# Kernel tuning notes

Measured on AMD Instinct MI355X. Metric: run time of the kernel, lower is better.

Reference implementation:

```python
import jax, jax.numpy as jnp
import numpy as np
import math

D_MODEL = 1024
NHEAD = 16
D_K = D_MODEL // NHEAD
B, S = 2, 2048


def setup_inputs() -> dict:
    key = jax.random.key(0)
    ks = jax.random.split(key, 9)
    x = jax.random.normal(ks[0], (B, S, D_MODEL), dtype=jnp.float32)
    # causal mask, broadcastable to (B, nhead, S, S); 0 entries are masked out
    mask = jnp.tril(jnp.ones((S, S), dtype=jnp.int32))[None, None, :, :]
    scale = 1.0 / math.sqrt(D_MODEL)
    def lin(kw, kb):
        W = jax.random.uniform(kw, (D_MODEL, D_MODEL), dtype=jnp.float32, minval=-scale, maxval=scale)
        b = jax.random.uniform(kb, (D_MODEL,), dtype=jnp.float32, minval=-scale, maxval=scale)
        return W, b
    Wq, bq = lin(ks[1], ks[2])
    Wk, bk = lin(ks[3], ks[4])
    Wv, bv = lin(ks[5], ks[6])
    Wo, bo = lin(ks[7], ks[8])
    return {"x": x, "mask": mask, "Wq": Wq, "bq": bq, "Wk": Wk, "bk": bk,
            "Wv": Wv, "bv": bv, "Wo": Wo, "bo": bo}


def reference(x, mask, Wq, bq, Wk, bk, Wv, bv, Wo, bo):
    b, s, _ = x.shape
    def heads(W, bias):
        # (b, s, d_model) @ (d_model, d_model) -> (b, nhead, s, d_k)
        return (x @ W.T + bias).reshape(b, s, NHEAD, D_K).transpose(0, 2, 1, 3)
    Q, K, V = heads(Wq, bq), heads(Wk, bk), heads(Wv, bv)
    scores = jnp.einsum('bhqd,bhkd->bhqk', Q, K) / math.sqrt(D_K)
    scores = jnp.where(mask == 0, jnp.float32(-1e9), scores)
    attn = jax.nn.softmax(scores, axis=-1)  # dropout is identity in eval mode
    out = jnp.einsum('bhqk,bhkd->bhqd', attn, V)
    out = out.transpose(0, 2, 1, 3).reshape(b, s, D_MODEL)
    return out @ Wo.T + bo
```

## Files before the change

kernel.cpp:

```cpp
#include <hip/hip_runtime.h>
#include <hip/hip_bf16.h>

#define DMODEL 1024
#define NH     16
#define DKH    64
#define BSZ    2
#define SEQ    2048
#define MROWS  (BSZ*SEQ)
#define WELEM  (DMODEL*DMODEL)

typedef __attribute__((ext_vector_type(8))) short short8;
typedef __attribute__((ext_vector_type(4))) float f32x4;

__device__ __forceinline__ ushort f2bf(float f) {
    return __bfloat16_as_ushort(__float2bfloat16(f));
}
__device__ __forceinline__ unsigned pk2(float lo, float hi) {
    return (unsigned)f2bf(lo) | ((unsigned)f2bf(hi) << 16);
}

__global__ __launch_bounds__(256)
void cvt_all(const float* __restrict__ x,
             const float* __restrict__ W0, const float* __restrict__ W1,
             const float* __restrict__ W2, const float* __restrict__ W3,
             ushort* __restrict__ xbf, ushort* __restrict__ Wcat,
             ushort* __restrict__ Wo)
{
    const int blk = blockIdx.x;
    const float* src;
    ushort* dst;
    int base;
    if (blk < 2048)      { src = x;  dst = xbf;             base = blk * 2048; }
    else if (blk < 2560) { src = W0; dst = Wcat;            base = (blk - 2048) * 2048; }
    else if (blk < 3072) { src = W1; dst = Wcat + WELEM;    base = (blk - 2560) * 2048; }
    else if (blk < 3584) { src = W2; dst = Wcat + 2*WELEM;  base = (blk - 3072) * 2048; }
    else                 { src = W3; dst = Wo;              base = (blk - 3584) * 2048; }
    const size_t off = (size_t)base + threadIdx.x * 8;
    const float4 f0 = *(const float4*)(src + off);
    const float4 f1 = *(const float4*)(src + off + 4);
    uint4 o;
    o.x = pk2(f0.x, f0.y); o.y = pk2(f0.z, f0.w);
    o.z = pk2(f1.x, f1.y); o.w = pk2(f1.z, f1.w);
    *(uint4*)(dst + off) = o;
}

__global__ __launch_bounds__(256)
void gemm_qkv(const ushort* __restrict__ xbf, const ushort* __restrict__ Wcat,
              const float* __restrict__ bq, const float* __restrict__ bk,
              const float* __restrict__ bv,
              ushort* __restrict__ Qh, ushort* __restrict__ Kh,
              ushort* __restrict__ VT)
{
    __shared__ ushort Ash[128][40];
    __shared__ ushort Bsh[128][40];

    const int t    = threadIdx.x;
    const int m0   = blockIdx.y * 128, n0 = blockIdx.x * 128;
    const int srow = t >> 1;
    const int shal = (t & 1) * 16;

    const int wave = t >> 6;
    const int lane = t & 63;
    const int wr   = (wave >> 1) * 64;
    const int wc   = (wave & 1) * 64;
    const int quad = lane >> 4;
    const int r16  = lane & 15;

    f32x4 acc[4][4];
    #pragma unroll
    for (int i = 0; i < 4; ++i)
        #pragma unroll
        for (int j = 0; j < 4; ++j)
            acc[i][j] = (f32x4){0.f, 0.f, 0.f, 0.f};

    for (int k0 = 0; k0 < DMODEL; k0 += 32) {
        const ushort* ap = xbf  + (size_t)(m0 + srow) * DMODEL + k0 + shal;
        const ushort* wp = Wcat + (size_t)(n0 + srow) * DMODEL + k0 + shal;
        *(uint4*)&Ash[srow][shal]     = *(const uint4*)(ap);
        *(uint4*)&Ash[srow][shal + 8] = *(const uint4*)(ap + 8);
        *(uint4*)&Bsh[srow][shal]     = *(const uint4*)(wp);
        *(uint4*)&Bsh[srow][shal + 8] = *(const uint4*)(wp + 8);
        __syncthreads();

        short8 af[4], bf[4];
        #pragma unroll
        for (int i = 0; i < 4; ++i) af[i] = *(const short8*)&Ash[wr + i * 16 + r16][quad * 8];
        #pragma unroll
        for (int j = 0; j < 4; ++j) bf[j] = *(const short8*)&Bsh[wc + j * 16 + r16][quad * 8];

        #pragma unroll
        for (int i = 0; i < 4; ++i)
            #pragma unroll
            for (int j = 0; j < 4; ++j)
                acc[i][j] = __builtin_amdgcn_mfma_f32_16x16x32_bf16(af[i], bf[j], acc[i][j], 0, 0, 0);
        __syncthreads();
    }

    const int region = n0 >> 10;
    const float* bp  = (region == 0) ? bq : (region == 1) ? bk : bv;
    ushort* outQK    = (region == 0) ? Qh : Kh;
    const float osc  = (region == 0) ? 0.125f : 1.0f;
    const int nbase  = n0 & 1023;

    #pragma unroll
    for (int i = 0; i < 4; ++i) {
        #pragma unroll
        for (int j = 0; j < 4; ++j) {
            #pragma unroll
            for (int reg = 0; reg < 4; ++reg) {
                const int m  = m0 + wr + i * 16 + quad * 4 + reg;
                const int n  = nbase + wc + j * 16 + r16;
                const float v = (acc[i][j][reg] + bp[n]) * osc;
                const int b = m >> 11, s = m & (SEQ - 1);
                const int h = n >> 6,  dk = n & 63;
                if (region < 2) {
                    outQK[((size_t)(b * NH + h) * SEQ + s) * DKH + dk] = f2bf(v);
                } else {
                    VT[(((size_t)(b * NH + h)) * DKH + dk) * SEQ + s] = f2bf(v);
                }
            }
        }
    }
}

__global__ __launch_bounds__(256)
void gemm_out(const ushort* __restrict__ O, const ushort* __restrict__ Wo,
              const float* __restrict__ bo, float* __restrict__ out)
{
    __shared__ ushort Ash[128][40];
    __shared__ ushort Bsh[64][40];

    const int t    = threadIdx.x;
    const int m0   = blockIdx.y * 128, n0 = blockIdx.x * 64;
    const int wave = t >> 6;
    const int lane = t & 63;
    const int wr   = (wave >> 1) * 64;
    const int wc   = (wave & 1) * 32;
    const int quad = lane >> 4;
    const int r16  = lane & 15;

    f32x4 acc[4][2];
    #pragma unroll
    for (int i = 0; i < 4; ++i)
        #pragma unroll
        for (int j = 0; j < 2; ++j)
            acc[i][j] = (f32x4){0.f, 0.f, 0.f, 0.f};

    for (int k0 = 0; k0 < DMODEL; k0 += 32) {
        {
            const int srow = t >> 1, shal = (t & 1) * 16;
            const int m = m0 + srow;
            const ushort* ap = O + ((size_t)(m >> 11) * NH + (k0 >> 6)) * (SEQ * DKH)
                                 + (size_t)(m & (SEQ - 1)) * DKH + (k0 & 63) + shal;
            *(uint4*)&Ash[srow][shal]     = *(const uint4*)(ap);
            *(uint4*)&Ash[srow][shal + 8] = *(const uint4*)(ap + 8);
        }
        {
            const int brow = t >> 2, bc = (t & 3) * 8;
            const ushort* wp = Wo + (size_t)(n0 + brow) * DMODEL + k0 + bc;
            *(uint4*)&Bsh[brow][bc] = *(const uint4*)(wp);
        }
        __syncthreads();

        short8 af[4], bf[2];
        #pragma unroll
        for (int i = 0; i < 4; ++i) af[i] = *(const short8*)&Ash[wr + i * 16 + r16][quad * 8];
        #pragma unroll
        for (int j = 0; j < 2; ++j) bf[j] = *(const short8*)&Bsh[wc + j * 16 + r16][quad * 8];

        #pragma unroll
        for (int i = 0; i < 4; ++i)
            #pragma unroll
            for (int j = 0; j < 2; ++j)
                acc[i][j] = __builtin_amdgcn_mfma_f32_16x16x32_bf16(af[i], bf[j], acc[i][j], 0, 0, 0);
        __syncthreads();
    }

    #pragma unroll
    for (int i = 0; i < 4; ++i) {
        #pragma unroll
        for (int j = 0; j < 2; ++j) {
            #pragma unroll
            for (int reg = 0; reg < 4; ++reg) {
                const int m = m0 + wr + i * 16 + quad * 4 + reg;
                const int n = n0 + wc + j * 16 + r16;
                out[(size_t)m * DMODEL + n] = acc[i][j][reg] + bo[n];
            }
        }
    }
}

__global__ __launch_bounds__(256)
void gemm_mfma(const void* __restrict__ A, const void* __restrict__ W,
               const float* __restrict__ bias, void* __restrict__ out,
               int amode, int bmode, int outmode, float oscale)
{
    __shared__ ushort Ash[128][40];
    __shared__ ushort Bsh[128][40];

    const int t    = threadIdx.x;
    const int m0   = blockIdx.y * 128, n0 = blockIdx.x * 128;
    const int srow = t >> 1;
    const int shal = (t & 1) * 16;

    const int wave = t >> 6;
    const int lane = t & 63;
    const int wr   = (wave >> 1) * 64;
    const int wc   = (wave & 1) * 64;
    const int quad = lane >> 4;
    const int r16  = lane & 15;

    f32x4 acc[4][4];
    #pragma unroll
    for (int i = 0; i < 4; ++i)
        #pragma unroll
        for (int j = 0; j < 4; ++j)
            acc[i][j] = (f32x4){0.f, 0.f, 0.f, 0.f};

    for (int k0 = 0; k0 < DMODEL; k0 += 32) {
        uint4 a01, a23, b01, b23;
        if (amode == 0) {
            const float* ap = (const float*)A + (size_t)(m0 + srow) * DMODEL + k0 + shal;
            const float4 f0 = *(const float4*)(ap);
            const float4 f1 = *(const float4*)(ap + 4);
            const float4 f2 = *(const float4*)(ap + 8);
            const float4 f3 = *(const float4*)(ap + 12);
            a01 = (uint4){pk2(f0.x,f0.y), pk2(f0.z,f0.w), pk2(f1.x,f1.y), pk2(f1.z,f1.w)};
            a23 = (uint4){pk2(f2.x,f2.y), pk2(f2.z,f2.w), pk2(f3.x,f3.y), pk2(f3.z,f3.w)};
        } else if (amode == 1) {
            const int m = m0 + srow;
            const ushort* ap = (const ushort*)A
                + ((size_t)(m >> 11) * NH + (k0 >> 6)) * (SEQ * DKH)
                + (size_t)(m & (SEQ - 1)) * DKH + (k0 & 63) + shal;
            a01 = *(const uint4*)(ap);
            a23 = *(const uint4*)(ap + 8);
        } else {
            const ushort* ap = (const ushort*)A + (size_t)(m0 + srow) * DMODEL + k0 + shal;
            a01 = *(const uint4*)(ap);
            a23 = *(const uint4*)(ap + 8);
        }
        if (bmode == 0) {
            const float* wp = (const float*)W + (size_t)(n0 + srow) * DMODEL + k0 + shal;
            const float4 w0 = *(const float4*)(wp);
            const float4 w1 = *(const float4*)(wp + 4);
            const float4 w2 = *(const float4*)(wp + 8);
            const float4 w3 = *(const float4*)(wp + 12);
            b01 = (uint4){pk2(w0.x,w0.y), pk2(w0.z,w0.w), pk2(w1.x,w1.y), pk2(w1.z,w1.w)};
            b23 = (uint4){pk2(w2.x,w2.y), pk2(w2.z,w2.w), pk2(w3.x,w3.y), pk2(w3.z,w3.w)};
        } else {
            const ushort* wp = (const ushort*)W + (size_t)(n0 + srow) * DMODEL + k0 + shal;
            b01 = *(const uint4*)(wp);
            b23 = *(const uint4*)(wp + 8);
        }

        *(uint4*)&Ash[srow][shal]     = a01;
        *(uint4*)&Ash[srow][shal + 8] = a23;
        *(uint4*)&Bsh[srow][shal]     = b01;
        *(uint4*)&Bsh[srow][shal + 8] = b23;
        __syncthreads();

        short8 af[4], bf[4];
        #pragma unroll
        for (int i = 0; i < 4; ++i) af[i] = *(const short8*)&Ash[wr + i * 16 + r16][quad * 8];
        #pragma unroll
        for (int j = 0; j < 4; ++j) bf[j] = *(const short8*)&Bsh[wc + j * 16 + r16][quad * 8];

        #pragma unroll
        for (int i = 0; i < 4; ++i)
            #pragma unroll
            for (int j = 0; j < 4; ++j)
                acc[i][j] = __builtin_amdgcn_mfma_f32_16x16x32_bf16(af[i], bf[j], acc[i][j], 0, 0, 0);
        __syncthreads();
    }

    #pragma unroll
    for (int i = 0; i < 4; ++i) {
        #pragma unroll
        for (int j = 0; j < 4; ++j) {
            #pragma unroll
            for (int reg = 0; reg < 4; ++reg) {
                const int m = m0 + wr + i * 16 + quad * 4 + reg;
                const int n = n0 + wc + j * 16 + r16;
                const float v = (acc[i][j][reg] + bias[n]) * oscale;
                if (outmode == 0) {
                    ((float*)out)[(size_t)m * DMODEL + n] = v;
                } else if (outmode == 1) {
                    ((ushort*)out)[((size_t)(m >> 11) * NH + (n >> 6)) * (SEQ * DKH)
                                   + (size_t)(m & (SEQ - 1)) * DKH + (n & 63)] = f2bf(v);
                } else {
                    ((ushort*)out)[(((size_t)(m >> 11) * NH + (n >> 6)) * DKH + (n & 63)) * SEQ
                                   + (m & (SEQ - 1))] = f2bf(v);
                }
            }
        }
    }
}

__global__ __launch_bounds__(256)
void attn_flash(ushort* __restrict__ Qh,
                const ushort* __restrict__ Kh,
                const ushort* __restrict__ VT)
{
    __shared__ ushort Kl[128][72];
    __shared__ ushort Vl[64][136];
    __shared__ ushort Pl[4][16][136];

    const int t256 = threadIdx.x;
    const int wave = t256 >> 6;
    const int lane = t256 & 63;
    const int quad = lane >> 4;
    const int r16  = lane & 15;

    const int slot = blockIdx.x & 7;
    const int rest = blockIdx.x >> 3;
    const int bh   = slot * 4 + (rest & 3);
    const int p    = rest >> 2;

    ushort*       Qbase = Qh + (size_t)bh * SEQ * DKH;
    const ushort* Kbase = Kh + (size_t)bh * SEQ * DKH;
    const ushort* Vbase = VT + (size_t)bh * DKH * SEQ;

    #pragma unroll
    for (int pass = 0; pass < 2; ++pass) {
        const int qt = pass ? (31 - p) : p;
        const int q0 = qt * 64;

        short8 qf[2];
        {
            const ushort* qrow = Qbase + (size_t)(q0 + wave * 16 + r16) * DKH;
            qf[0] = *(const short8*)(qrow + quad * 8);
            qf[1] = *(const short8*)(qrow + 32 + quad * 8);
        }

        f32x4 oacc[4];
        #pragma unroll
        for (int i = 0; i < 4; ++i) oacc[i] = (f32x4){0.f, 0.f, 0.f, 0.f};
        float lpart[4] = {0.f, 0.f, 0.f, 0.f};

        const int T   = (qt >> 1) + 1;
        const int off = (qt & 1) * 64;

        for (int t = 0; t < T; ++t) {
            {
                const int krow = t256 >> 1, kc = (t256 & 1) * 32;
                const ushort* kg = Kbase + (size_t)(t * 128 + krow) * DKH + kc;
                *(uint4*)&Kl[krow][kc]      = *(const uint4*)(kg);
                *(uint4*)&Kl[krow][kc + 8]  = *(const uint4*)(kg + 8);
                *(uint4*)&Kl[krow][kc + 16] = *(const uint4*)(kg + 16);
                *(uint4*)&Kl[krow][kc + 24] = *(const uint4*)(kg + 24);
                const int vrow = t256 >> 2, vc = (t256 & 3) * 32;
                const ushort* vg = Vbase + (size_t)vrow * SEQ + t * 128 + vc;
                *(uint4*)&Vl[vrow][vc]      = *(const uint4*)(vg);
                *(uint4*)&Vl[vrow][vc + 8]  = *(const uint4*)(vg + 8);
                *(uint4*)&Vl[vrow][vc + 16] = *(const uint4*)(vg + 16);
                *(uint4*)&Vl[vrow][vc + 24] = *(const uint4*)(vg + 24);
            }
            __syncthreads();

            f32x4 sacc[8];
            #pragma unroll
            for (int nt = 0; nt < 8; ++nt) {
                sacc[nt] = (f32x4){0.f, 0.f, 0.f, 0.f};
                short8 b0 = *(const short8*)&Kl[nt * 16 + r16][quad * 8];
                short8 b1 = *(const short8*)&Kl[nt * 16 + r16][32 + quad * 8];
                sacc[nt] = __builtin_amdgcn_mfma_f32_16x16x32_bf16(qf[0], b0, sacc[nt], 0, 0, 0);
                sacc[nt] = __builtin_amdgcn_mfma_f32_16x16x32_bf16(qf[1], b1, sacc[nt], 0, 0, 0);
            }

            const bool diag = (t == T - 1);
            #pragma unroll
            for (int reg = 0; reg < 4; ++reg) {
                const int row_local = wave * 16 + quad * 4 + reg + off;
                #pragma unroll
                for (int nt = 0; nt < 8; ++nt) {
                    float pv = __expf(sacc[nt][reg]);
                    if (diag && (nt * 16 + r16) > row_local) pv = 0.f;
                    lpart[reg] += pv;
                    Pl[wave][quad * 4 + reg][nt * 16 + r16] = f2bf(pv);
                }
            }

            #pragma unroll
            for (int c = 0; c < 4; ++c) {
                short8 af = *(const short8*)&Pl[wave][r16][c * 32 + quad * 8];
                #pragma unroll
                for (int ct = 0; ct < 4; ++ct) {
                    short8 bf = *(const short8*)&Vl[ct * 16 + r16][c * 32 + quad * 8];
                    oacc[ct] = __builtin_amdgcn_mfma_f32_16x16x32_bf16(af, bf, oacc[ct], 0, 0, 0);
                }
            }
            __syncthreads();
        }

        #pragma unroll
        for (int reg = 0; reg < 4; ++reg)
            for (int d = 1; d < 16; d <<= 1)
                lpart[reg] += __shfl_xor(lpart[reg], d, 64);

        #pragma unroll
        for (int reg = 0; reg < 4; ++reg) {
            const float inv = 1.f / lpart[reg];
            const int q = q0 + wave * 16 + quad * 4 + reg;
            ushort* orow = Qbase + (size_t)q * DKH;
            #pragma unroll
            for (int ct = 0; ct < 4; ++ct)
                orow[ct * 16 + r16] = f2bf(oacc[ct][reg] * inv);
        }
        __syncthreads();
    }
}

extern "C" void kernel_launch(void* const* d_in, const int* in_sizes, int n_in,
                              void* d_out, int out_size, void* d_ws, size_t ws_size,
                              hipStream_t stream)
{
    const float* x  = (const float*)d_in[0];
    const float* Wf[4] = {(const float*)d_in[2], (const float*)d_in[4],
                          (const float*)d_in[6], (const float*)d_in[8]};
    const float* Bf[4] = {(const float*)d_in[3], (const float*)d_in[5],
                          (const float*)d_in[7], (const float*)d_in[9]};

    const size_t HSZ = (size_t)MROWS * DMODEL;
    ushort* Qh = (ushort*)d_ws;
    ushort* Kh = (ushort*)d_out;
    ushort* VT = (ushort*)d_out + HSZ;

    const dim3 blk(256);

    if (ws_size >= 24u * 1024 * 1024) {
        ushort* Wcat = Qh + HSZ;
        ushort* Wo   = Wcat + 3 * (size_t)WELEM;
        ushort* xbf  = Wo + WELEM;

        cvt_all<<<dim3(4096), blk, 0, stream>>>(x, Wf[0], Wf[1], Wf[2], Wf[3],
                                                xbf, Wcat, Wo);

        gemm_qkv<<<dim3(3 * DMODEL / 128, MROWS / 128), blk, 0, stream>>>(
            xbf, Wcat, Bf[0], Bf[1], Bf[2], Qh, Kh, VT);

        attn_flash<<<dim3(BSZ * NH * 16), blk, 0, stream>>>(Qh, Kh, VT);

        gemm_out<<<dim3(DMODEL / 64, MROWS / 128), blk, 0, stream>>>(
            Qh, Wo, Bf[3], (float*)d_out);
    } else {
        const dim3 gg(DMODEL / 128, MROWS / 128);
        gemm_mfma<<<gg, blk, 0, stream>>>(x, Wf[0], Bf[0], Qh, 0, 0, 1, 0.125f);
        gemm_mfma<<<gg, blk, 0, stream>>>(x, Wf[1], Bf[1], Kh, 0, 0, 1, 1.0f);
        gemm_mfma<<<gg, blk, 0, stream>>>(x, Wf[2], Bf[2], VT, 0, 0, 2, 1.0f);
        attn_flash<<<dim3(BSZ * NH * 16), blk, 0, stream>>>(Qh, Kh, VT);
        gemm_mfma<<<gg, blk, 0, stream>>>(Qh, Wf[3], Bf[3], d_out, 1, 0, 0, 1.0f);
    }
}
```

Baseline: 217.3 us.

## Use direct global-to-LDS loads in GEMMs and one query tile per attention block

Both GEMM kernels now stage their tiles with global_load_lds, which writes global memory straight into LDS without passing through registers. The LDS rows lose their padding, so the MFMA fragment reads may hit more bank conflicts. Separately, the attention kernel drops the paired-pass scheme where each block handled tile p and tile 31-p. It now launches twice as many blocks, one query tile each, trading the old load balancing for more parallelism and fewer registers live across passes.

```diff
diff --git a/kernel.cpp b/kernel.cpp
--- a/kernel.cpp
+++ b/kernel.cpp
@@ -17,6 +17,11 @@
 }
 __device__ __forceinline__ unsigned pk2(float lo, float hi) {
     return (unsigned)f2bf(lo) | ((unsigned)f2bf(hi) << 16);
+}
+__device__ __forceinline__ void load_lds16(const ushort* g, ushort* l) {
+    __builtin_amdgcn_global_load_lds(
+        (const __attribute__((address_space(1))) unsigned int*)g,
+        (__attribute__((address_space(3))) unsigned int*)l, 16, 0, 0);
 }
 
 __global__ __launch_bounds__(256)
@@ -51,14 +56,11 @@
               ushort* __restrict__ Qh, ushort* __restrict__ Kh,
               ushort* __restrict__ VT)
 {
-    __shared__ ushort Ash[128][40];
-    __shared__ ushort Bsh[128][40];
+    __shared__ ushort Ash[128][32];
+    __shared__ ushort Bsh[128][32];
 
     const int t    = threadIdx.x;
     const int m0   = blockIdx.y * 128, n0 = blockIdx.x * 128;
-    const int srow = t >> 1;
-    const int shal = (t & 1) * 16;
-
     const int wave = t >> 6;
     const int lane = t & 63;
     const int wr   = (wave >> 1) * 64;
@@ -66,6 +68,10 @@
     const int quad = lane >> 4;
     const int r16  = lane & 15;
 
+    const int row0 = wave * 16 + (lane >> 2);
+    const int row1 = 64 + wave * 16 + (lane >> 2);
+    const int ch   = (lane & 3) * 8;
+
     f32x4 acc[4][4];
     #pragma unroll
     for (int i = 0; i < 4; ++i)
@@ -74,12 +80,10 @@
             acc[i][j] = (f32x4){0.f, 0.f, 0.f, 0.f};
 
     for (int k0 = 0; k0 < DMODEL; k0 += 32) {
-        const ushort* ap = xbf  + (size_t)(m0 + srow) * DMODEL + k0 + shal;
-        const ushort* wp = Wcat + (size_t)(n0 + srow) * DMODEL + k0 + shal;
-        *(uint4*)&Ash[srow][shal]     = *(const uint4*)(ap);
-        *(uint4*)&Ash[srow][shal + 8] = *(const uint4*)(ap + 8);
-        *(uint4*)&Bsh[srow][shal]     = *(const uint4*)(wp);
-        *(uint4*)&Bsh[srow][shal + 8] = *(const uint4*)(wp + 8);
+        load_lds16(xbf  + (size_t)(m0 + row0) * DMODEL + k0 + ch, &Ash[wave * 16][0]);
+        load_lds16(xbf  + (size_t)(m0 + row1) * DMODEL + k0 + ch, &Ash[64 + wave * 16][0]);
+        load_lds16(Wcat + (size_t)(n0 + row0) * DMODEL + k0 + ch, &Bsh[wave * 16][0]);
+        load_lds16(Wcat + (size_t)(n0 + row1) * DMODEL + k0 + ch, &Bsh[64 + wave * 16][0]);
         __syncthreads();
 
         short8 af[4], bf[4];
@@ -127,8 +131,8 @@
 void gemm_out(const ushort* __restrict__ O, const ushort* __restrict__ Wo,
               const float* __restrict__ bo, float* __restrict__ out)
 {
-    __shared__ ushort Ash[128][40];
-    __shared__ ushort Bsh[64][40];
+    __shared__ ushort Ash[128][32];
+    __shared__ ushort Bsh[64][32];
 
     const int t    = threadIdx.x;
     const int m0   = blockIdx.y * 128, n0 = blockIdx.x * 64;
@@ -139,6 +143,10 @@
     const int quad = lane >> 4;
     const int r16  = lane & 15;
 
+    const int row0 = wave * 16 + (lane >> 2);
+    const int row1 = 64 + wave * 16 + (lane >> 2);
+    const int ch   = (lane & 3) * 8;
+
     f32x4 acc[4][2];
     #pragma unroll
     for (int i = 0; i < 4; ++i)
@@ -147,19 +155,14 @@
             acc[i][j] = (f32x4){0.f, 0.f, 0.f, 0.f};
 
     for (int k0 = 0; k0 < DMODEL; k0 += 32) {
-        {
-            const int srow = t >> 1, shal = (t & 1) * 16;
-            const int m = m0 + srow;
-            const ushort* ap = O + ((size_t)(m >> 11) * NH + (k0 >> 6)) * (SEQ * DKH)
-                                 + (size_t)(m & (SEQ - 1)) * DKH + (k0 & 63) + shal;
-            *(uint4*)&Ash[srow][shal]     = *(const uint4*)(ap);
-            *(uint4*)&Ash[srow][shal + 8] = *(const uint4*)(ap + 8);
-        }
-        {
-            const int brow = t >> 2, bc = (t & 3) * 8;
-            const ushort* wp = Wo + (size_t)(n0 + brow) * DMODEL + k0 + bc;
-            *(uint4*)&Bsh[brow][bc] = *(const uint4*)(wp);
-        }
+        const int ma0 = m0 + row0, ma1 = m0 + row1;
+        load_lds16(O + ((size_t)(ma0 >> 11) * NH + (k0 >> 6)) * (SEQ * DKH)
+                     + (size_t)(ma0 & (SEQ - 1)) * DKH + (k0 & 63) + ch,
+                   &Ash[wave * 16][0]);
+        load_lds16(O + ((size_t)(ma1 >> 11) * NH + (k0 >> 6)) * (SEQ * DKH)
+                     + (size_t)(ma1 & (SEQ - 1)) * DKH + (k0 & 63) + ch,
+                   &Ash[64 + wave * 16][0]);
+        load_lds16(Wo + (size_t)(n0 + row0) * DMODEL + k0 + ch, &Bsh[wave * 16][0]);
         __syncthreads();
 
         short8 af[4], bf[2];
@@ -312,101 +315,94 @@
     const int r16  = lane & 15;
 
     const int slot = blockIdx.x & 7;
-    const int rest = blockIdx.x >> 3;
-    const int bh   = slot * 4 + (rest & 3);
-    const int p    = rest >> 2;
+    const int bh   = slot * 4 + ((blockIdx.x >> 3) & 3);
+    const int qt   = blockIdx.x >> 5;
+    const int q0   = qt * 64;
 
     ushort*       Qbase = Qh + (size_t)bh * SEQ * DKH;
     const ushort* Kbase = Kh + (size_t)bh * SEQ * DKH;
     const ushort* Vbase = VT + (size_t)bh * DKH * SEQ;
 
-    #pragma unroll
-    for (int pass = 0; pass < 2; ++pass) {
-        const int qt = pass ? (31 - p) : p;
-        const int q0 = qt * 64;
-
-        short8 qf[2];
+    short8 qf[2];
+    {
+        const ushort* qrow = Qbase + (size_t)(q0 + wave * 16 + r16) * DKH;
+        qf[0] = *(const short8*)(qrow + quad * 8);
+        qf[1] = *(const short8*)(qrow + 32 + quad * 8);
+    }
+
+    f32x4 oacc[4];
+    #pragma unroll
+    for (int i = 0; i < 4; ++i) oacc[i] = (f32x4){0.f, 0.f, 0.f, 0.f};
+    float lpart[4] = {0.f, 0.f, 0.f, 0.f};
+
+    const int T   = (qt >> 1) + 1;
+    const int off = (qt & 1) * 64;
+
+    for (int t = 0; t < T; ++t) {
         {
-            const ushort* qrow = Qbase + (size_t)(q0 + wave * 16 + r16) * DKH;
-            qf[0] = *(const short8*)(qrow + quad * 8);
-            qf[1] = *(const short8*)(qrow + 32 + quad * 8);
-        }
-
-        f32x4 oacc[4];
-        #pragma unroll
-        for (int i = 0; i < 4; ++i) oacc[i] = (f32x4){0.f, 0.f, 0.f, 0.f};
-        float lpart[4] = {0.f, 0.f, 0.f, 0.f};
-
-        const int T   = (qt >> 1) + 1;
-        const int off = (qt & 1) * 64;
-
-        for (int t = 0; t < T; ++t) {
-            {
-                const int krow = t256 >> 1, kc = (t256 & 1) * 32;
-                const ushort* kg = Kbase + (size_t)(t * 128 + krow) * DKH + kc;
-                *(uint4*)&Kl[krow][kc]      = *(const uint4*)(kg);
-                *(uint4*)&Kl[krow][kc + 8]  = *(const uint4*)(kg + 8);
-                *(uint4*)&Kl[krow][kc + 16] = *(const uint4*)(kg + 16);
-                *(uint4*)&Kl[krow][kc + 24] = *(const uint4*)(kg + 24);
-                const int vrow = t256 >> 2, vc = (t256 & 3) * 32;
-                const ushort* vg = Vbase + (size_t)vrow * SEQ + t * 128 + vc;
-                *(uint4*)&Vl[vrow][vc]      = *(const uint4*)(vg);
-                *(uint4*)&Vl[vrow][vc + 8]  = *(const uint4*)(vg + 8);
-                *(uint4*)&Vl[vrow][vc + 16] = *(const uint4*)(vg + 16);
-                *(uint4*)&Vl[vrow][vc + 24] = *(const uint4*)(vg + 24);
+            const int krow = t256 >> 1, kc = (t256 & 1) * 32;
+            const ushort* kg = Kbase + (size_t)(t * 128 + krow) * DKH + kc;
+            *(uint4*)&Kl[krow][kc]      = *(const uint4*)(kg);
+            *(uint4*)&Kl[krow][kc + 8]  = *(const uint4*)(kg + 8);
+            *(uint4*)&Kl[krow][kc + 16] = *(const uint4*)(kg + 16);
+            *(uint4*)&Kl[krow][kc + 24] = *(const uint4*)(kg + 24);
+            const int vrow = t256 >> 2, vc = (t256 & 3) * 32;
+            const ushort* vg = Vbase + (size_t)vrow * SEQ + t * 128 + vc;
+            *(uint4*)&Vl[vrow][vc]      = *(const uint4*)(vg);
+            *(uint4*)&Vl[vrow][vc + 8]  = *(const uint4*)(vg + 8);
+            *(uint4*)&Vl[vrow][vc + 16] = *(const uint4*)(vg + 16);
+            *(uint4*)&Vl[vrow][vc + 24] = *(const uint4*)(vg + 24);
+        }
+        __syncthreads();
+
+        f32x4 sacc[8];
+        #pragma unroll
+        for (int nt = 0; nt < 8; ++nt) {
+            sacc[nt] = (f32x4){0.f, 0.f, 0.f, 0.f};
+            short8 b0 = *(const short8*)&Kl[nt * 16 + r16][quad * 8];
+            short8 b1 = *(const short8*)&Kl[nt * 16 + r16][32 + quad * 8];
+            sacc[nt] = __builtin_amdgcn_mfma_f32_16x16x32_bf16(qf[0], b0, sacc[nt], 0, 0, 0);
+            sacc[nt] = __builtin_amdgcn_mfma_f32_16x16x32_bf16(qf[1], b1, sacc[nt], 0, 0, 0);
+        }
+
+        const bool diag = (t == T - 1);
+        #pragma unroll
+        for (int reg = 0; reg < 4; ++reg) {
+            const int row_local = wave * 16 + quad * 4 + reg + off;
+            #pragma unroll
+            for (int nt = 0; nt < 8; ++nt) {
+                float pv = __expf(sacc[nt][reg]);
+                if (diag && (nt * 16 + r16) > row_local) pv = 0.f;
+                lpart[reg] += pv;
+                Pl[wave][quad * 4 + reg][nt * 16 + r16] = f2bf(pv);
             }
-            __syncthreads();
-
-            f32x4 sacc[8];
-            #pragma unroll
-            for (int nt = 0; nt < 8; ++nt) {
-                sacc[nt] = (f32x4){0.f, 0.f, 0.f, 0.f};
-                short8 b0 = *(const short8*)&Kl[nt * 16 + r16][quad * 8];
-                short8 b1 = *(const short8*)&Kl[nt * 16 + r16][32 + quad * 8];
-                sacc[nt] = __builtin_amdgcn_mfma_f32_16x16x32_bf16(qf[0], b0, sacc[nt], 0, 0, 0);
-                sacc[nt] = __builtin_amdgcn_mfma_f32_16x16x32_bf16(qf[1], b1, sacc[nt], 0, 0, 0);
+        }
+
+        #pragma unroll
+        for (int c = 0; c < 4; ++c) {
+            short8 af = *(const short8*)&Pl[wave][r16][c * 32 + quad * 8];
+            #pragma unroll
+            for (int ct = 0; ct < 4; ++ct) {
+                short8 bf = *(const short8*)&Vl[ct * 16 + r16][c * 32 + quad * 8];
+                oacc[ct] = __builtin_amdgcn_mfma_f32_16x16x32_bf16(af, bf, oacc[ct], 0, 0, 0);
             }
-
-            const bool diag = (t == T - 1);
-            #pragma unroll
-            for (int reg = 0; reg < 4; ++reg) {
-                const int row_local = wave * 16 + quad * 4 + reg + off;
-                #pragma unroll
-                for (int nt = 0; nt < 8; ++nt) {
-                    float pv = __expf(sacc[nt][reg]);
-                    if (diag && (nt * 16 + r16) > row_local) pv = 0.f;
-                    lpart[reg] += pv;
-                    Pl[wave][quad * 4 + reg][nt * 16 + r16] = f2bf(pv);
-                }
-            }
-
-            #pragma unroll
-            for (int c = 0; c < 4; ++c) {
-                short8 af = *(const short8*)&Pl[wave][r16][c * 32 + quad * 8];
-                #pragma unroll
-                for (int ct = 0; ct < 4; ++ct) {
-                    short8 bf = *(const short8*)&Vl[ct * 16 + r16][c * 32 + quad * 8];
-                    oacc[ct] = __builtin_amdgcn_mfma_f32_16x16x32_bf16(af, bf, oacc[ct], 0, 0, 0);
-                }
-            }
-            __syncthreads();
-        }
-
-        #pragma unroll
-        for (int reg = 0; reg < 4; ++reg)
-            for (int d = 1; d < 16; d <<= 1)
-                lpart[reg] += __shfl_xor(lpart[reg], d, 64);
-
-        #pragma unroll
-        for (int reg = 0; reg < 4; ++reg) {
-            const float inv = 1.f / lpart[reg];
-            const int q = q0 + wave * 16 + quad * 4 + reg;
-            ushort* orow = Qbase + (size_t)q * DKH;
-            #pragma unroll
-            for (int ct = 0; ct < 4; ++ct)
-                orow[ct * 16 + r16] = f2bf(oacc[ct][reg] * inv);
-        }
-        __syncthreads();
+        }
+        __syncthreads();
+    }
+
+    #pragma unroll
+    for (int reg = 0; reg < 4; ++reg)
+        for (int d = 1; d < 16; d <<= 1)
+            lpart[reg] += __shfl_xor(lpart[reg], d, 64);
+
+    #pragma unroll
+    for (int reg = 0; reg < 4; ++reg) {
+        const float inv = 1.f / lpart[reg];
+        const int q = q0 + wave * 16 + quad * 4 + reg;
+        ushort* orow = Qbase + (size_t)q * DKH;
+        #pragma unroll
+        for (int ct = 0; ct < 4; ++ct)
+            orow[ct * 16 + r16] = f2bf(oacc[ct][reg] * inv);
     }
 }
 
@@ -438,7 +434,7 @@
         gemm_qkv<<<dim3(3 * DMODEL / 128, MROWS / 128), blk, 0, stream>>>(
             xbf, Wcat, Bf[0], Bf[1], Bf[2], Qh, Kh, VT);
 
-        attn_flash<<<dim3(BSZ * NH * 16), blk, 0, stream>>>(Qh, Kh, VT);
+        attn_flash<<<dim3(BSZ * NH * 32), blk, 0, stream>>>(Qh, Kh, VT);
 
         gemm_out<<<dim3(DMODEL / 64, MROWS / 128), blk, 0, stream>>>(
             Qh, Wo, Bf[3], (float*)d_out);
@@ -447,7 +443,7 @@
         gemm_mfma<<<gg, blk, 0, stream>>>(x, Wf[0], Bf[0], Qh, 0, 0, 1, 0.125f);
         gemm_mfma<<<gg, blk, 0, stream>>>(x, Wf[1], Bf[1], Kh, 0, 0, 1, 1.0f);
         gemm_mfma<<<gg, blk, 0, stream>>>(x, Wf[2], Bf[2], VT, 0, 0, 2, 1.0f);
-        attn_flash<<<dim3(BSZ * NH * 16), blk, 0, stream>>>(Qh, Kh, VT);
+        attn_flash<<<dim3(BSZ * NH * 32), blk, 0, stream>>>(Qh, Kh, VT);
         gemm_mfma<<<gg, blk, 0, stream>>>(Qh, Wf[3], Bf[3], d_out, 1, 0, 0, 1.0f);
     }
 }
```

Result: no change. 214.1 us (-1.4%).
